# Kernel optimization log

Measured on AMD Instinct MI355X. Metric: run time of the kernel, lower is better.

## Reference

```python
import jax, jax.numpy as jnp
import numpy as np

N_NODES = 50000
N_EDGES = 1600000
IN_CH = 128
HID = 32
HEADS = 4
N_LAYERS = 3
NEG_SLOPE = 0.2


def setup_inputs() -> dict:
    key = jax.random.key(0)
    ks = jax.random.split(key, 2 + 6 * N_LAYERS)
    inp = {
        "x": jax.random.normal(ks[0], (N_NODES, IN_CH), dtype=jnp.float32),
        "edge_index": jax.random.randint(ks[1], (2, N_EDGES), 0, N_NODES, dtype=jnp.int64),
    }
    HC = HID * HEADS  # 128, equals IN_CH so all layers share shapes
    for l in range(N_LAYERS):
        fan_in = IN_CH if l == 0 else HC
        s = 1.0 / np.sqrt(fan_in)
        k = ks[2 + 6 * l: 2 + 6 * (l + 1)]
        inp[f"Wl{l}"] = jax.random.normal(k[0], (fan_in, HC), dtype=jnp.float32) * s
        inp[f"bl{l}"] = jnp.zeros((HC,), dtype=jnp.float32)
        inp[f"Wr{l}"] = jax.random.normal(k[1], (fan_in, HC), dtype=jnp.float32) * s
        inp[f"br{l}"] = jnp.zeros((HC,), dtype=jnp.float32)
        inp[f"att{l}"] = jax.random.normal(k[2], (HEADS, HID), dtype=jnp.float32) * (1.0 / np.sqrt(HID))
        inp[f"b{l}"] = jnp.zeros((HC,), dtype=jnp.float32)
    return inp


def gatv2_layer(x, src, dst, Wl, bl, Wr, br, att, b):
    # GATv2Conv: xl = lin_l(x) for source msgs, xr = lin_r(x) for targets
    xl = (x @ Wl + bl).reshape(N_NODES, HEADS, HID)
    xr = (x @ Wr + br).reshape(N_NODES, HEADS, HID)
    h = xl[src] + xr[dst]                                   # [E, H, C] gather
    e = jnp.sum(att * jax.nn.leaky_relu(h, NEG_SLOPE), -1)  # [E, H] per-edge score
    # segment softmax over incoming edges of each dst node
    m = jax.ops.segment_max(e, dst, num_segments=N_NODES)   # [N, H]
    w = jnp.exp(e - m[dst])
    z = jax.ops.segment_sum(w, dst, num_segments=N_NODES)
    alpha = w / z[dst]                                      # [E, H]
    out = jax.ops.segment_sum(alpha[..., None] * xl[src], dst, num_segments=N_NODES)
    return out.reshape(N_NODES, HEADS * HID) + b


def reference(x, edge_index, Wl0, bl0, Wr0, br0, att0, b0,
              Wl1, bl1, Wr1, br1, att1, b1,
              Wl2, bl2, Wr2, br2, att2, b2):
    # add self loops (PyG GATv2Conv default add_self_loops=True)
    loops = jnp.arange(N_NODES, dtype=edge_index.dtype)
    src = jnp.concatenate([edge_index[0], loops])
    dst = jnp.concatenate([edge_index[1], loops])
    params = [(Wl0, bl0, Wr0, br0, att0, b0),
              (Wl1, bl1, Wr1, br1, att1, b1),
              (Wl2, bl2, Wr2, br2, att2, b2)]
    for i, p in enumerate(params):
        x = gatv2_layer(x, src, dst, *p)
        if i < N_LAYERS - 1:
            x = jax.nn.elu(x)  # dropout p=0.0 / eval mode -> identity
    return x
```

## Files before the change

### kernel.cpp

```cpp
#include <hip/hip_runtime.h>
#include <hip/hip_fp16.h>
#include <math.h>

#define N_NODES 50000
#define N_EDGES 1600000
#define ETOT (N_EDGES + N_NODES)
#define HC 128
#define HEADS 4
#define HID 32
#define NEG_SLOPE 0.2f
#define NPB 32
#define NBUCKETS ((N_NODES + NPB - 1) / NPB)
#define CHUNK 8192
#define NCHUNK ((ETOT + CHUNK - 1) / CHUNK)
#define LOG2E 1.4426950408889634f
#define NEGBIG (-1e30f)

typedef _Float16 h2 __attribute__((ext_vector_type(2)));

__device__ __forceinline__ unsigned pack2(float a, float b) {
    return ((unsigned)__half_as_ushort(__float2half(b)) << 16) | __half_as_ushort(__float2half(a));
}

__device__ __forceinline__ float fdot2u(unsigned a, unsigned b, float c) {
#if __has_builtin(__builtin_amdgcn_fdot2)
    return __builtin_amdgcn_fdot2(__builtin_bit_cast(h2, a), __builtin_bit_cast(h2, b), c, false);
#else
    h2 ha = __builtin_bit_cast(h2, a);
    h2 hb = __builtin_bit_cast(h2, b);
    return fmaf((float)ha[0], (float)hb[0], fmaf((float)ha[1], (float)hb[1], c));
#endif
}


__global__ __launch_bounds__(256) void bucket_hist_kernel(const int* __restrict__ dstArr,
                                                          int* __restrict__ bucketCount) {
    __shared__ int hist[NBUCKETS];
    int c0 = blockIdx.x * CHUNK;
    int c1 = min(c0 + CHUNK, ETOT);
    for (int b = threadIdx.x; b < NBUCKETS; b += 256) hist[b] = 0;
    __syncthreads();
    for (int i = c0 + threadIdx.x; i < c1; i += 256) {
        int d = (i < N_EDGES) ? dstArr[i] : (i - N_EDGES);
        atomicAdd(&hist[d >> 5], 1);
    }
    __syncthreads();
    for (int b = threadIdx.x; b < NBUCKETS; b += 256) {
        int h = hist[b];
        if (h > 0) atomicAdd(&bucketCount[b], h);
    }
}

__global__ __launch_bounds__(1024) void bucket_scan_kernel(const int* __restrict__ bucketCount,
                                                           int* __restrict__ bucketStart,
                                                           int* __restrict__ bucketCursor,
                                                           int* __restrict__ rowStart) {
    __shared__ int buf[1024];
    __shared__ int carry;
    if (threadIdx.x == 0) carry = 0;
    __syncthreads();
    for (int base = 0; base < NBUCKETS; base += 1024) {
        int i = base + threadIdx.x;
        int v = (i < NBUCKETS) ? bucketCount[i] : 0;
        buf[threadIdx.x] = v;
        __syncthreads();
        for (int off = 1; off < 1024; off <<= 1) {
            int t = (threadIdx.x >= off) ? buf[threadIdx.x - off] : 0;
            __syncthreads();
            buf[threadIdx.x] += t;
            __syncthreads();
        }
        if (i < NBUCKETS) {
            int excl = carry + buf[threadIdx.x] - v;
            bucketStart[i] = excl;
            bucketCursor[i] = excl;
        }
        __syncthreads();
        if (threadIdx.x == 1023) carry += buf[1023];
        __syncthreads();
    }
    if (threadIdx.x == 0) {
        bucketStart[NBUCKETS] = ETOT;
        rowStart[N_NODES] = ETOT;
    }
}

__global__ __launch_bounds__(256) void chunk_scatter_kernel(const int* __restrict__ srcArr, const int* __restrict__ dstArr,
                                                            int* __restrict__ bucketCursor, int* __restrict__ E) {
    __shared__ int hist[NBUCKETS];
    int c0 = blockIdx.x * CHUNK;
    int c1 = min(c0 + CHUNK, ETOT);
    for (int b = threadIdx.x; b < NBUCKETS; b += 256) hist[b] = 0;
    __syncthreads();

    int myP[CHUNK / 256];
    int cnt = 0;
    for (int i = c0 + threadIdx.x; i < c1; i += 256) {
        int s, d;
        if (i < N_EDGES) { s = srcArr[i]; d = dstArr[i]; }
        else             { s = i - N_EDGES; d = s; }
        myP[cnt] = s | (d << 16);
        cnt++;
        atomicAdd(&hist[d >> 5], 1);
    }
    __syncthreads();
    for (int b = threadIdx.x; b < NBUCKETS; b += 256) {
        int h = hist[b];
        hist[b] = (h > 0) ? atomicAdd(&bucketCursor[b], h) : 0;
    }
    __syncthreads();
    for (int k = 0; k < cnt; k++) {
        int pe = myP[k];
        int pos = atomicAdd(&hist[((unsigned)pe) >> 21], 1);
        E[pos] = pe;
    }
}

__global__ __launch_bounds__(256) void csr_scatter_kernel(const int* __restrict__ E,
                                                          const int* __restrict__ bucketStart,
                                                          int* __restrict__ rowStart,
                                                          int* __restrict__ srcOff) {
    __shared__ int cnt[NPB];
    __shared__ int lcur[NPB];
    int b = blockIdx.x;
    int n0 = b * NPB;
    int e0 = bucketStart[b];
    int e1 = bucketStart[b + 1];
    if (threadIdx.x < NPB) cnt[threadIdx.x] = 0;
    __syncthreads();
    for (int i = e0 + threadIdx.x; i < e1; i += 256)
        atomicAdd(&cnt[(E[i] >> 16) & (NPB - 1)], 1);
    __syncthreads();
    if (threadIdx.x == 0) {
        int run = e0;
#pragma unroll
        for (int j = 0; j < NPB; j++) {
            lcur[j] = run;
            int n = n0 + j;
            if (n < N_NODES) rowStart[n] = run;
            run += cnt[j];
        }
    }
    __syncthreads();
    for (int i = e0 + threadIdx.x; i < e1; i += 256) {
        int pe = E[i];
        int pos = atomicAdd(&lcur[(pe >> 16) & (NPB - 1)], 1);
        srcOff[pos] = (pe & 0xFFFF) << 8;
    }
}


__global__ __launch_bounds__(256) void cvt_x_kernel(const float* __restrict__ x, __half* __restrict__ xh) {
    int i = blockIdx.x * 256 + threadIdx.x;
    if (i >= N_NODES * HC / 8) return;
    const float4* s = reinterpret_cast<const float4*>(x + (size_t)i * 8);
    float4 v0 = s[0], v1 = s[1];
    uint4 o;
    o.x = pack2(v0.x, v0.y); o.y = pack2(v0.z, v0.w);
    o.z = pack2(v1.x, v1.y); o.w = pack2(v1.z, v1.w);
    reinterpret_cast<uint4*>(xh)[i] = o;
}

__global__ __launch_bounds__(256) void pack_w_kernel(const float* __restrict__ Wl, const float* __restrict__ Wr,
                                                     unsigned* __restrict__ Wp) {
    int i = blockIdx.x * 256 + threadIdx.x;
    if (i >= 2 * 64 * HC) return;
    int mat = i >> 13;
    int k2 = (i >> 7) & 63;
    int n = i & 127;
    const float* W = mat ? Wr : Wl;
    Wp[i] = pack2(W[(2 * k2) * HC + n], W[(2 * k2 + 1) * HC + n]);
}


__global__ __launch_bounds__(256) void gemm_kernel(const __half* __restrict__ xin,
    const unsigned* __restrict__ Wp, const float* __restrict__ bl, const float* __restrict__ br,
    __half* __restrict__ XLh, float* __restrict__ XR) {
    __shared__ unsigned As2[128][20];
    __shared__ unsigned Bs2[16][132];
    int t = threadIdx.x;
    int rb = blockIdx.x * 128;
    int mat = blockIdx.y;
    const float* bias = mat ? br : bl;
    int tx = t & 15, ty = t >> 4;

    float acc00[4][4], acc01[4][4], acc10[4][4], acc11[4][4];
#pragma unroll
    for (int i = 0; i < 4; i++)
#pragma unroll
        for (int j = 0; j < 4; j++) { acc00[i][j] = 0.f; acc01[i][j] = 0.f; acc10[i][j] = 0.f; acc11[i][j] = 0.f; }

    for (int kt = 0; kt < 4; kt++) {
#pragma unroll
        for (int it = 0; it < 2; it++) {
            int idx = it * 256 + t;
            int r = idx >> 2, f = idx & 3;
            int gr = rb + r;
            uint4 v = make_uint4(0, 0, 0, 0);
            if (gr < N_NODES) v = *reinterpret_cast<const uint4*>(xin + (size_t)gr * HC + kt * 32 + f * 8);
            *reinterpret_cast<uint4*>(&As2[r][f * 4]) = v;
        }
#pragma unroll
        for (int it = 0; it < 2; it++) {
            int idx = it * 256 + t;
            int k2 = idx >> 5, f = idx & 31;
            *reinterpret_cast<uint4*>(&Bs2[k2][f * 4]) =
                *reinterpret_cast<const uint4*>(Wp + ((size_t)(mat * 64 + kt * 16 + k2) * HC + f * 4));
        }
        __syncthreads();
#pragma unroll
        for (int k2 = 0; k2 < 16; k2++) {
            uint4 bv0 = *reinterpret_cast<const uint4*>(&Bs2[k2][tx * 4]);
            uint4 bv1 = *reinterpret_cast<const uint4*>(&Bs2[k2][64 + tx * 4]);
            unsigned av[8];
#pragma unroll
            for (int i = 0; i < 4; i++) av[i] = As2[ty * 4 + i][k2];
#pragma unroll
            for (int i = 0; i < 4; i++) av[4 + i] = As2[64 + ty * 4 + i][k2];
#pragma unroll
            for (int i = 0; i < 4; i++) {
                acc00[i][0] = fdot2u(av[i], bv0.x, acc00[i][0]);
                acc00[i][1] = fdot2u(av[i], bv0.y, acc00[i][1]);
                acc00[i][2] = fdot2u(av[i], bv0.z, acc00[i][2]);
                acc00[i][3] = fdot2u(av[i], bv0.w, acc00[i][3]);
                acc01[i][0] = fdot2u(av[i], bv1.x, acc01[i][0]);
                acc01[i][1] = fdot2u(av[i], bv1.y, acc01[i][1]);
                acc01[i][2] = fdot2u(av[i], bv1.z, acc01[i][2]);
                acc01[i][3] = fdot2u(av[i], bv1.w, acc01[i][3]);
                acc10[i][0] = fdot2u(av[4 + i], bv0.x, acc10[i][0]);
                acc10[i][1] = fdot2u(av[4 + i], bv0.y, acc10[i][1]);
                acc10[i][2] = fdot2u(av[4 + i], bv0.z, acc10[i][2]);
                acc10[i][3] = fdot2u(av[4 + i], bv0.w, acc10[i][3]);
                acc11[i][0] = fdot2u(av[4 + i], bv1.x, acc11[i][0]);
                acc11[i][1] = fdot2u(av[4 + i], bv1.y, acc11[i][1]);
                acc11[i][2] = fdot2u(av[4 + i], bv1.z, acc11[i][2]);
                acc11[i][3] = fdot2u(av[4 + i], bv1.w, acc11[i][3]);
            }
        }
        __syncthreads();
    }

    float4 bb0 = *reinterpret_cast<const float4*>(&bias[tx * 4]);
    float4 bb1 = *reinterpret_cast<const float4*>(&bias[64 + tx * 4]);
#pragma unroll
    for (int i = 0; i < 4; i++) {
        int gr0 = rb + ty * 4 + i;
        int gr1 = rb + 64 + ty * 4 + i;
        float4 o00, o01, o10, o11;
        o00.x = acc00[i][0] + bb0.x; o00.y = acc00[i][1] + bb0.y; o00.z = acc00[i][2] + bb0.z; o00.w = acc00[i][3] + bb0.w;
        o01.x = acc01[i][0] + bb1.x; o01.y = acc01[i][1] + bb1.y; o01.z = acc01[i][2] + bb1.z; o01.w = acc01[i][3] + bb1.w;
        o10.x = acc10[i][0] + bb0.x; o10.y = acc10[i][1] + bb0.y; o10.z = acc10[i][2] + bb0.z; o10.w = acc10[i][3] + bb0.w;
        o11.x = acc11[i][0] + bb1.x; o11.y = acc11[i][1] + bb1.y; o11.z = acc11[i][2] + bb1.z; o11.w = acc11[i][3] + bb1.w;
        if (mat == 0) {
            if (gr0 < N_NODES) {
                uint2 u0, u1;
                u0.x = pack2(o00.x, o00.y); u0.y = pack2(o00.z, o00.w);
                u1.x = pack2(o01.x, o01.y); u1.y = pack2(o01.z, o01.w);
                *reinterpret_cast<uint2*>(&XLh[(size_t)gr0 * HC + tx * 4]) = u0;
                *reinterpret_cast<uint2*>(&XLh[(size_t)gr0 * HC + 64 + tx * 4]) = u1;
            }
            if (gr1 < N_NODES) {
                uint2 u0, u1;
                u0.x = pack2(o10.x, o10.y); u0.y = pack2(o10.z, o10.w);
                u1.x = pack2(o11.x, o11.y); u1.y = pack2(o11.z, o11.w);
                *reinterpret_cast<uint2*>(&XLh[(size_t)gr1 * HC + tx * 4]) = u0;
                *reinterpret_cast<uint2*>(&XLh[(size_t)gr1 * HC + 64 + tx * 4]) = u1;
            }
        } else {
            if (gr0 < N_NODES) {
                *reinterpret_cast<float4*>(&XR[(size_t)gr0 * HC + tx * 4]) = o00;
                *reinterpret_cast<float4*>(&XR[(size_t)gr0 * HC + 64 + tx * 4]) = o01;
            }
            if (gr1 < N_NODES) {
                *reinterpret_cast<float4*>(&XR[(size_t)gr1 * HC + tx * 4]) = o10;
                *reinterpret_cast<float4*>(&XR[(size_t)gr1 * HC + 64 + tx * 4]) = o11;
            }
        }
    }
}


__device__ __forceinline__ float score8p(uint4 xl, const unsigned* __restrict__ xrh,
                                         const unsigned* __restrict__ ah) {
    const h2 slope = { (_Float16)NEG_SLOPE, (_Float16)NEG_SLOPE };
    unsigned u[4] = { xl.x, xl.y, xl.z, xl.w };
    float c = 0.f;
#pragma unroll
    for (int j = 0; j < 4; j++) {
        h2 s = __builtin_bit_cast(h2, u[j]) + __builtin_bit_cast(h2, xrh[j]);
        h2 t = s * slope;
        h2 m = __builtin_elementwise_max(s, t);
        c = fdot2u(__builtin_bit_cast(unsigned, m), ah[j], c);
    }
    c += __shfl_xor(c, 1);
    c += __shfl_xor(c, 2);
    return fminf(c, 120.f);
}

__device__ __forceinline__ void upd8p(float c, uint4 xl, float& z, float* __restrict__ acc) {
    float w = exp2f(c);
    z += w;
    unsigned u[4] = { xl.x, xl.y, xl.z, xl.w };
#pragma unroll
    for (int j = 0; j < 4; j++) {
        h2 h = __builtin_bit_cast(h2, u[j]);
        acc[2 * j]     = fmaf(w, (float)h[0], acc[2 * j]);
        acc[2 * j + 1] = fmaf(w, (float)h[1], acc[2 * j + 1]);
    }
}

__global__ __launch_bounds__(256) void gat_fused_kernel(const __half* __restrict__ XLh,
    const float* __restrict__ XR, const float* __restrict__ att,
    const int* __restrict__ rowStart, const int* __restrict__ srcOff,
    const float* __restrict__ bvec, float* __restrict__ outF, __half* __restrict__ outH,
    int applyElu) {
    int wv = threadIdx.x >> 6;
    int l = threadIdx.x & 63;
    int q = l >> 4;
    int cl = l & 15;
    int n = blockIdx.x * 4 + wv;
    if (n >= N_NODES) return;
    int s0 = rowStart[n], s1 = rowStart[n + 1];

    unsigned xrh[4], ah[4];
    {
        float4 x0 = *reinterpret_cast<const float4*>(&XR[(size_t)n * HC + 8 * cl]);
        float4 x1 = *reinterpret_cast<const float4*>(&XR[(size_t)n * HC + 8 * cl + 4]);
        float4 a0 = *reinterpret_cast<const float4*>(&att[8 * cl]);
        float4 a1 = *reinterpret_cast<const float4*>(&att[8 * cl + 4]);
        xrh[0] = pack2(x0.x, x0.y); xrh[1] = pack2(x0.z, x0.w);
        xrh[2] = pack2(x1.x, x1.y); xrh[3] = pack2(x1.z, x1.w);
        ah[0] = pack2(a0.x * LOG2E, a0.y * LOG2E); ah[1] = pack2(a0.z * LOG2E, a0.w * LOG2E);
        ah[2] = pack2(a1.x * LOG2E, a1.y * LOG2E); ah[3] = pack2(a1.z * LOG2E, a1.w * LOG2E);
    }
    const char* XLb = reinterpret_cast<const char*>(XLh) + 16 * cl;

    float z = 0.f;
    float acc[8];
#pragma unroll
    for (int i = 0; i < 8; i++) acc[i] = 0.f;

    int p = s0;
    for (; p + 16 <= s1; p += 16) {
        int oA = srcOff[p      + q];
        int oB = srcOff[p + 4  + q];
        int oC = srcOff[p + 8  + q];
        int oD = srcOff[p + 12 + q];
        uint4 xA = *reinterpret_cast<const uint4*>(XLb + (size_t)(unsigned)oA);
        uint4 xB = *reinterpret_cast<const uint4*>(XLb + (size_t)(unsigned)oB);
        uint4 xC = *reinterpret_cast<const uint4*>(XLb + (size_t)(unsigned)oC);
        uint4 xD = *reinterpret_cast<const uint4*>(XLb + (size_t)(unsigned)oD);
        float cA = score8p(xA, xrh, ah);
        float cB = score8p(xB, xrh, ah);
        float cC = score8p(xC, xrh, ah);
        float cD = score8p(xD, xrh, ah);
        upd8p(cA, xA, z, acc);
        upd8p(cB, xB, z, acc);
        upd8p(cC, xC, z, acc);
        upd8p(cD, xD, z, acc);
    }
    for (; p + 4 <= s1; p += 4) {
        int o = srcOff[p + q];
        uint4 x = *reinterpret_cast<const uint4*>(XLb + (size_t)(unsigned)o);
        float c = score8p(x, xrh, ah);
        upd8p(c, x, z, acc);
    }
    if (p < s1) {
        int r = s1 - p;
        int o = srcOff[min(p + q, s1 - 1)];
        uint4 x = *reinterpret_cast<const uint4*>(XLb + (size_t)(unsigned)o);
        float c = score8p(x, xrh, ah);
        if (q >= r) c = NEGBIG;
        upd8p(c, x, z, acc);
    }

    z += __shfl_xor(z, 16);
    z += __shfl_xor(z, 32);
#pragma unroll
    for (int i = 0; i < 8; i++) {
        acc[i] += __shfl_xor(acc[i], 16);
        acc[i] += __shfl_xor(acc[i], 32);
    }

    if (q == 0) {
        float zinv = 1.f / z;
        float4 b0 = *reinterpret_cast<const float4*>(&bvec[8 * cl]);
        float4 b1 = *reinterpret_cast<const float4*>(&bvec[8 * cl + 4]);
        float o0[8];
        o0[0] = acc[0] * zinv + b0.x; o0[1] = acc[1] * zinv + b0.y;
        o0[2] = acc[2] * zinv + b0.z; o0[3] = acc[3] * zinv + b0.w;
        o0[4] = acc[4] * zinv + b1.x; o0[5] = acc[5] * zinv + b1.y;
        o0[6] = acc[6] * zinv + b1.z; o0[7] = acc[7] * zinv + b1.w;
        if (applyElu) {
#pragma unroll
            for (int i = 0; i < 8; i++) o0[i] = o0[i] > 0.f ? o0[i] : (__expf(o0[i]) - 1.f);
        }
        if (outH) {
            uint4 u;
            u.x = pack2(o0[0], o0[1]); u.y = pack2(o0[2], o0[3]);
            u.z = pack2(o0[4], o0[5]); u.w = pack2(o0[6], o0[7]);
            *reinterpret_cast<uint4*>(&outH[(size_t)n * HC + 8 * cl]) = u;
        } else {
            *reinterpret_cast<float4*>(&outF[(size_t)n * HC + 8 * cl]) = make_float4(o0[0], o0[1], o0[2], o0[3]);
            *reinterpret_cast<float4*>(&outF[(size_t)n * HC + 8 * cl + 4]) = make_float4(o0[4], o0[5], o0[6], o0[7]);
        }
    }
}


extern "C" void kernel_launch(void* const* d_in, const int* in_sizes, int n_in,
                              void* d_out, int out_size, void* d_ws, size_t ws_size,
                              hipStream_t stream) {
    const float* x = (const float*)d_in[0];
    const int* ei = (const int*)d_in[1];
    const int* srcArr = ei;
    const int* dstArr = ei + N_EDGES;

    char* ws = (char*)d_ws;
    size_t off = 0;
    auto alloc = [&](size_t bytes) -> void* {
        void* p = ws + off;
        off = (off + bytes + 511) & ~(size_t)511;
        return p;
    };
    __half* xh      = (__half*)alloc((size_t)N_NODES * HC * 2);
    __half* Ph      = (__half*)alloc((size_t)N_NODES * HC * 2);
    __half* XLh     = (__half*)alloc((size_t)N_NODES * HC * 2);
    float* XR       = (float*)alloc((size_t)N_NODES * HC * 4);
    unsigned* Wp    = (unsigned*)alloc((size_t)2 * 64 * HC * 4);
    int* rowStart   = (int*)alloc((size_t)(N_NODES + 1) * 4);
    int* bucketCnt  = (int*)alloc((size_t)NBUCKETS * 4);
    int* bucketStart= (int*)alloc((size_t)(NBUCKETS + 1) * 4);
    int* bucketCur  = (int*)alloc((size_t)NBUCKETS * 4);
    int* E          = (int*)alloc((size_t)ETOT * 4);
    int* srcOff     = (int*)alloc((size_t)ETOT * 4);

    (void)hipMemsetAsync(bucketCnt, 0, (size_t)NBUCKETS * 4, stream);
    bucket_hist_kernel<<<NCHUNK, 256, 0, stream>>>(dstArr, bucketCnt);
    bucket_scan_kernel<<<1, 1024, 0, stream>>>(bucketCnt, bucketStart, bucketCur, rowStart);
    chunk_scatter_kernel<<<NCHUNK, 256, 0, stream>>>(srcArr, dstArr, bucketCur, E);
    csr_scatter_kernel<<<NBUCKETS, 256, 0, stream>>>(E, bucketStart, rowStart, srcOff);
    cvt_x_kernel<<<(N_NODES * HC / 8 + 255) / 256, 256, 0, stream>>>(x, xh);

    for (int lyr = 0; lyr < 3; lyr++) {
        const __half* gin = (lyr == 0) ? xh : Ph;
        const float* Wl  = (const float*)d_in[2 + 6 * lyr + 0];
        const float* bl  = (const float*)d_in[2 + 6 * lyr + 1];
        const float* Wr  = (const float*)d_in[2 + 6 * lyr + 2];
        const float* br  = (const float*)d_in[2 + 6 * lyr + 3];
        const float* att = (const float*)d_in[2 + 6 * lyr + 4];
        const float* bb  = (const float*)d_in[2 + 6 * lyr + 5];

        pack_w_kernel<<<(2 * 64 * HC + 255) / 256, 256, 0, stream>>>(Wl, Wr, Wp);

        dim3 ggrid((N_NODES + 127) / 128, 2);
        gemm_kernel<<<ggrid, 256, 0, stream>>>(gin, Wp, bl, br, XLh, XR);

        int nb = (N_NODES + 3) / 4;
        gat_fused_kernel<<<nb, 256, 0, stream>>>(XLh, XR, att, rowStart, srcOff, bb,
                                                 lyr == 2 ? (float*)d_out : nullptr,
                                                 lyr < 2 ? Ph : nullptr,
                                                 lyr < 2 ? 1 : 0);
    }
}
```

Measured before the change: 374.2 us.

## Merge prep kernels into one launch and store XR in fp16

Fuses x conversion, all three layers' weight packing, attention-vector packing and the bucket histogram into one prep kernel launch. This removes five small launches and the per-layer pack_w launches. The GEMM now writes XR as fp16 instead of fp32, which halves its write traffic and the per-node read in the fused GAT kernel. The GAT kernel also loads pre-scaled packed attention weights instead of converting them per node. XR was already rounded to fp16 inside the GAT kernel before this change, so accuracy should be essentially unchanged.

```diff
diff --git a/kernel.cpp b/kernel.cpp
--- a/kernel.cpp
+++ b/kernel.cpp
@@ -16,6 +16,10 @@
 #define LOG2E 1.4426950408889634f
 #define NEGBIG (-1e30f)
 
+#define CVTB (N_NODES * HC / 8 / 256)
+#define WB   (3 * 2 * 64 * HC / 256)
+#define PREPB (CVTB + WB + 1 + NCHUNK)
+
 typedef _Float16 h2 __attribute__((ext_vector_type(2)));
 
 __device__ __forceinline__ unsigned pack2(float a, float b) {
@@ -33,21 +37,64 @@
 }
 
 
-__global__ __launch_bounds__(256) void bucket_hist_kernel(const int* __restrict__ dstArr,
-                                                          int* __restrict__ bucketCount) {
-    __shared__ int hist[NBUCKETS];
-    int c0 = blockIdx.x * CHUNK;
-    int c1 = min(c0 + CHUNK, ETOT);
-    for (int b = threadIdx.x; b < NBUCKETS; b += 256) hist[b] = 0;
-    __syncthreads();
-    for (int i = c0 + threadIdx.x; i < c1; i += 256) {
-        int d = (i < N_EDGES) ? dstArr[i] : (i - N_EDGES);
-        atomicAdd(&hist[d >> 5], 1);
-    }
-    __syncthreads();
-    for (int b = threadIdx.x; b < NBUCKETS; b += 256) {
-        int h = hist[b];
-        if (h > 0) atomicAdd(&bucketCount[b], h);
+__global__ __launch_bounds__(256) void prep_kernel(const float* __restrict__ x, __half* __restrict__ xh,
+    const float* __restrict__ Wl0, const float* __restrict__ Wr0,
+    const float* __restrict__ Wl1, const float* __restrict__ Wr1,
+    const float* __restrict__ Wl2, const float* __restrict__ Wr2,
+    const float* __restrict__ att0, const float* __restrict__ att1, const float* __restrict__ att2,
+    unsigned* __restrict__ Wp, unsigned* __restrict__ attp,
+    const int* __restrict__ dstArr, int* __restrict__ bucketCount) {
+    int b = blockIdx.x;
+    if (b < CVTB) {
+        int i = b * 256 + threadIdx.x;
+        const float4* s = reinterpret_cast<const float4*>(x + (size_t)i * 8);
+        float4 v0 = s[0], v1 = s[1];
+        uint4 o;
+        o.x = pack2(v0.x, v0.y); o.y = pack2(v0.z, v0.w);
+        o.z = pack2(v1.x, v1.y); o.w = pack2(v1.z, v1.w);
+        reinterpret_cast<uint4*>(xh)[i] = o;
+        return;
+    }
+    b -= CVTB;
+    if (b < WB) {
+        int i = b * 256 + threadIdx.x;
+        int lyr = i >> 14;
+        int rem = i & 16383;
+        int mat = rem >> 13;
+        int k2 = (rem >> 7) & 63;
+        int n = rem & 127;
+        const float* Ws[6] = { Wl0, Wr0, Wl1, Wr1, Wl2, Wr2 };
+        const float* W = Ws[lyr * 2 + mat];
+        Wp[i] = pack2(W[(2 * k2) * HC + n], W[(2 * k2 + 1) * HC + n]);
+        return;
+    }
+    b -= WB;
+    if (b < 1) {
+        int i = threadIdx.x;
+        if (i < 3 * 64) {
+            int lyr = i >> 6;
+            int j = i & 63;
+            const float* as[3] = { att0, att1, att2 };
+            attp[i] = pack2(as[lyr][2 * j] * LOG2E, as[lyr][2 * j + 1] * LOG2E);
+        }
+        return;
+    }
+    b -= 1;
+    {
+        __shared__ int hist[NBUCKETS];
+        int c0 = b * CHUNK;
+        int c1 = min(c0 + CHUNK, ETOT);
+        for (int k = threadIdx.x; k < NBUCKETS; k += 256) hist[k] = 0;
+        __syncthreads();
+        for (int i = c0 + threadIdx.x; i < c1; i += 256) {
+            int d = (i < N_EDGES) ? dstArr[i] : (i - N_EDGES);
+            atomicAdd(&hist[d >> 5], 1);
+        }
+        __syncthreads();
+        for (int k = threadIdx.x; k < NBUCKETS; k += 256) {
+            int h = hist[k];
+            if (h > 0) atomicAdd(&bucketCount[k], h);
+        }
     }
 }
 
@@ -150,38 +197,16 @@
 }
 
 
-__global__ __launch_bounds__(256) void cvt_x_kernel(const float* __restrict__ x, __half* __restrict__ xh) {
-    int i = blockIdx.x * 256 + threadIdx.x;
-    if (i >= N_NODES * HC / 8) return;
-    const float4* s = reinterpret_cast<const float4*>(x + (size_t)i * 8);
-    float4 v0 = s[0], v1 = s[1];
-    uint4 o;
-    o.x = pack2(v0.x, v0.y); o.y = pack2(v0.z, v0.w);
-    o.z = pack2(v1.x, v1.y); o.w = pack2(v1.z, v1.w);
-    reinterpret_cast<uint4*>(xh)[i] = o;
-}
-
-__global__ __launch_bounds__(256) void pack_w_kernel(const float* __restrict__ Wl, const float* __restrict__ Wr,
-                                                     unsigned* __restrict__ Wp) {
-    int i = blockIdx.x * 256 + threadIdx.x;
-    if (i >= 2 * 64 * HC) return;
-    int mat = i >> 13;
-    int k2 = (i >> 7) & 63;
-    int n = i & 127;
-    const float* W = mat ? Wr : Wl;
-    Wp[i] = pack2(W[(2 * k2) * HC + n], W[(2 * k2 + 1) * HC + n]);
-}
-
-
 __global__ __launch_bounds__(256) void gemm_kernel(const __half* __restrict__ xin,
     const unsigned* __restrict__ Wp, const float* __restrict__ bl, const float* __restrict__ br,
-    __half* __restrict__ XLh, float* __restrict__ XR) {
+    __half* __restrict__ XLh, __half* __restrict__ XRh) {
     __shared__ unsigned As2[128][20];
     __shared__ unsigned Bs2[16][132];
     int t = threadIdx.x;
     int rb = blockIdx.x * 128;
     int mat = blockIdx.y;
     const float* bias = mat ? br : bl;
+    __half* dst = mat ? XRh : XLh;
     int tx = t & 15, ty = t >> 4;
 
     float acc00[4][4], acc01[4][4], acc10[4][4], acc11[4][4];
@@ -246,35 +271,23 @@
     for (int i = 0; i < 4; i++) {
         int gr0 = rb + ty * 4 + i;
         int gr1 = rb + 64 + ty * 4 + i;
-        float4 o00, o01, o10, o11;
-        o00.x = acc00[i][0] + bb0.x; o00.y = acc00[i][1] + bb0.y; o00.z = acc00[i][2] + bb0.z; o00.w = acc00[i][3] + bb0.w;
-        o01.x = acc01[i][0] + bb1.x; o01.y = acc01[i][1] + bb1.y; o01.z = acc01[i][2] + bb1.z; o01.w = acc01[i][3] + bb1.w;
-        o10.x = acc10[i][0] + bb0.x; o10.y = acc10[i][1] + bb0.y; o10.z = acc10[i][2] + bb0.z; o10.w = acc10[i][3] + bb0.w;
-        o11.x = acc11[i][0] + bb1.x; o11.y = acc11[i][1] + bb1.y; o11.z = acc11[i][2] + bb1.z; o11.w = acc11[i][3] + bb1.w;
-        if (mat == 0) {
-            if (gr0 < N_NODES) {
-                uint2 u0, u1;
-                u0.x = pack2(o00.x, o00.y); u0.y = pack2(o00.z, o00.w);
-                u1.x = pack2(o01.x, o01.y); u1.y = pack2(o01.z, o01.w);
-                *reinterpret_cast<uint2*>(&XLh[(size_t)gr0 * HC + tx * 4]) = u0;
-                *reinterpret_cast<uint2*>(&XLh[(size_t)gr0 * HC + 64 + tx * 4]) = u1;
-            }
-            if (gr1 < N_NODES) {
-                uint2 u0, u1;
-                u0.x = pack2(o10.x, o10.y); u0.y = pack2(o10.z, o10.w);
-                u1.x = pack2(o11.x, o11.y); u1.y = pack2(o11.z, o11.w);
-                *reinterpret_cast<uint2*>(&XLh[(size_t)gr1 * HC + tx * 4]) = u0;
-                *reinterpret_cast<uint2*>(&XLh[(size_t)gr1 * HC + 64 + tx * 4]) = u1;
-            }
-        } else {
-            if (gr0 < N_NODES) {
-                *reinterpret_cast<float4*>(&XR[(size_t)gr0 * HC + tx * 4]) = o00;
-                *reinterpret_cast<float4*>(&XR[(size_t)gr0 * HC + 64 + tx * 4]) = o01;
-            }
-            if (gr1 < N_NODES) {
-                *reinterpret_cast<float4*>(&XR[(size_t)gr1 * HC + tx * 4]) = o10;
-                *reinterpret_cast<float4*>(&XR[(size_t)gr1 * HC + 64 + tx * 4]) = o11;
-            }
+        if (gr0 < N_NODES) {
+            uint2 u0, u1;
+            u0.x = pack2(acc00[i][0] + bb0.x, acc00[i][1] + bb0.y);
+            u0.y = pack2(acc00[i][2] + bb0.z, acc00[i][3] + bb0.w);
+            u1.x = pack2(acc01[i][0] + bb1.x, acc01[i][1] + bb1.y);
+            u1.y = pack2(acc01[i][2] + bb1.z, acc01[i][3] + bb1.w);
+            *reinterpret_cast<uint2*>(&dst[(size_t)gr0 * HC + tx * 4]) = u0;
+            *reinterpret_cast<uint2*>(&dst[(size_t)gr0 * HC + 64 + tx * 4]) = u1;
+        }
+        if (gr1 < N_NODES) {
+            uint2 u0, u1;
+            u0.x = pack2(acc10[i][0] + bb0.x, acc10[i][1] + bb0.y);
+            u0.y = pack2(acc10[i][2] + bb0.z, acc10[i][3] + bb0.w);
+            u1.x = pack2(acc11[i][0] + bb1.x, acc11[i][1] + bb1.y);
+            u1.y = pack2(acc11[i][2] + bb1.z, acc11[i][3] + bb1.w);
+            *reinterpret_cast<uint2*>(&dst[(size_t)gr1 * HC + tx * 4]) = u0;
+            *reinterpret_cast<uint2*>(&dst[(size_t)gr1 * HC + 64 + tx * 4]) = u1;
         }
     }
 }
@@ -310,7 +323,7 @@
 }
 
 __global__ __launch_bounds__(256) void gat_fused_kernel(const __half* __restrict__ XLh,
-    const float* __restrict__ XR, const float* __restrict__ att,
+    const __half* __restrict__ XRh, const unsigned* __restrict__ attp,
     const int* __restrict__ rowStart, const int* __restrict__ srcOff,
     const float* __restrict__ bvec, float* __restrict__ outF, __half* __restrict__ outH,
     int applyElu) {
@@ -322,17 +335,10 @@
     if (n >= N_NODES) return;
     int s0 = rowStart[n], s1 = rowStart[n + 1];
 
-    unsigned xrh[4], ah[4];
-    {
-        float4 x0 = *reinterpret_cast<const float4*>(&XR[(size_t)n * HC + 8 * cl]);
-        float4 x1 = *reinterpret_cast<const float4*>(&XR[(size_t)n * HC + 8 * cl + 4]);
-        float4 a0 = *reinterpret_cast<const float4*>(&att[8 * cl]);
-        float4 a1 = *reinterpret_cast<const float4*>(&att[8 * cl + 4]);
-        xrh[0] = pack2(x0.x, x0.y); xrh[1] = pack2(x0.z, x0.w);
-        xrh[2] = pack2(x1.x, x1.y); xrh[3] = pack2(x1.z, x1.w);
-        ah[0] = pack2(a0.x * LOG2E, a0.y * LOG2E); ah[1] = pack2(a0.z * LOG2E, a0.w * LOG2E);
-        ah[2] = pack2(a1.x * LOG2E, a1.y * LOG2E); ah[3] = pack2(a1.z * LOG2E, a1.w * LOG2E);
-    }
+    uint4 xrv = *reinterpret_cast<const uint4*>(XRh + (size_t)n * HC + 8 * cl);
+    uint4 av  = *reinterpret_cast<const uint4*>(attp + 4 * cl);
+    unsigned xrh[4] = { xrv.x, xrv.y, xrv.z, xrv.w };
+    unsigned ah[4]  = { av.x, av.y, av.z, av.w };
     const char* XLb = reinterpret_cast<const char*>(XLh) + 16 * cl;
 
     float z = 0.f;
@@ -426,8 +432,9 @@
     __half* xh      = (__half*)alloc((size_t)N_NODES * HC * 2);
     __half* Ph      = (__half*)alloc((size_t)N_NODES * HC * 2);
     __half* XLh     = (__half*)alloc((size_t)N_NODES * HC * 2);
-    float* XR       = (float*)alloc((size_t)N_NODES * HC * 4);
-    unsigned* Wp    = (unsigned*)alloc((size_t)2 * 64 * HC * 4);
+    __half* XRh     = (__half*)alloc((size_t)N_NODES * HC * 2);
+    unsigned* Wp    = (unsigned*)alloc((size_t)3 * 2 * 64 * HC * 4);
+    unsigned* attp  = (unsigned*)alloc((size_t)3 * 64 * 4);
     int* rowStart   = (int*)alloc((size_t)(N_NODES + 1) * 4);
     int* bucketCnt  = (int*)alloc((size_t)NBUCKETS * 4);
     int* bucketStart= (int*)alloc((size_t)(NBUCKETS + 1) * 4);
@@ -436,28 +443,27 @@
     int* srcOff     = (int*)alloc((size_t)ETOT * 4);
 
     (void)hipMemsetAsync(bucketCnt, 0, (size_t)NBUCKETS * 4, stream);
-    bucket_hist_kernel<<<NCHUNK, 256, 0, stream>>>(dstArr, bucketCnt);
+    prep_kernel<<<PREPB, 256, 0, stream>>>(x, xh,
+        (const float*)d_in[2], (const float*)d_in[4],
+        (const float*)d_in[8], (const float*)d_in[10],
+        (const float*)d_in[14], (const float*)d_in[16],
+        (const float*)d_in[6], (const float*)d_in[12], (const float*)d_in[18],
+        Wp, attp, dstArr, bucketCnt);
     bucket_scan_kernel<<<1, 1024, 0, stream>>>(bucketCnt, bucketStart, bucketCur, rowStart);
     chunk_scatter_kernel<<<NCHUNK, 256, 0, stream>>>(srcArr, dstArr, bucketCur, E);
     csr_scatter_kernel<<<NBUCKETS, 256, 0, stream>>>(E, bucketStart, rowStart, srcOff);
-    cvt_x_kernel<<<(N_NODES * HC / 8 + 255) / 256, 256, 0, stream>>>(x, xh);
 
     for (int lyr = 0; lyr < 3; lyr++) {
         const __half* gin = (lyr == 0) ? xh : Ph;
-        const float* Wl  = (const float*)d_in[2 + 6 * lyr + 0];
         const float* bl  = (const float*)d_in[2 + 6 * lyr + 1];
-        const float* Wr  = (const float*)d_in[2 + 6 * lyr + 2];
         const float* br  = (const float*)d_in[2 + 6 * lyr + 3];
-        const float* att = (const float*)d_in[2 + 6 * lyr + 4];
         const float* bb  = (const float*)d_in[2 + 6 * lyr + 5];
 
-        pack_w_kernel<<<(2 * 64 * HC + 255) / 256, 256, 0, stream>>>(Wl, Wr, Wp);
-
         dim3 ggrid((N_NODES + 127) / 128, 2);
-        gemm_kernel<<<ggrid, 256, 0, stream>>>(gin, Wp, bl, br, XLh, XR);
+        gemm_kernel<<<ggrid, 256, 0, stream>>>(gin, Wp + (size_t)lyr * 2 * 64 * HC, bl, br, XLh, XRh);
 
         int nb = (N_NODES + 3) / 4;
-        gat_fused_kernel<<<nb, 256, 0, stream>>>(XLh, XR, att, rowStart, srcOff, bb,
+        gat_fused_kernel<<<nb, 256, 0, stream>>>(XLh, XRh, attp + lyr * 64, rowStart, srcOff, bb,
                                                  lyr == 2 ? (float*)d_out : nullptr,
                                                  lyr < 2 ? Ph : nullptr,
                                                  lyr < 2 ? 1 : 0);
```

After: 363.0 us. -3.0%, faster.
